# Kernel tuning notes

Measured on AMD Instinct MI355X. Metric: run time of the kernel, lower is better.

The kernel has to match this reference:

```python
import jax, jax.numpy as jnp
import numpy as np

B = 16384          # batch
F = 256            # num_features
H1, H2 = 32, 16    # hidden_units


def setup_inputs() -> dict:
    key = jax.random.key(0)
    ks = jax.random.split(key, 7)
    return {
        "x":  jax.random.normal(ks[0], (B, F), dtype=jnp.float32),
        "W1": jax.random.normal(ks[1], (F, 1, H1), dtype=jnp.float32) * 0.5,
        "b1": jax.random.normal(ks[2], (F, H1), dtype=jnp.float32) * 0.1,
        "W2": jax.random.normal(ks[3], (F, H1, H2), dtype=jnp.float32) * (1.0 / np.sqrt(H1)),
        "b2": jax.random.normal(ks[4], (F, H2), dtype=jnp.float32) * 0.1,
        "W3": jax.random.normal(ks[5], (F, H2, 1), dtype=jnp.float32) * (1.0 / np.sqrt(H2)),
        "b3": jax.random.normal(ks[6], (F, 1), dtype=jnp.float32) * 0.1,
    }


def reference(x, W1, b1, W2, b2, W3, b3):
    # Per-feature tiny MLP 1->H1->H2->1, batched over features as grouped GEMMs.
    # x: [B, F] (each feature is a scalar input to its own network)
    h1 = jax.nn.relu(jnp.einsum('bf,fh->bfh', x, W1[:, 0, :]) + b1)          # [B,F,H1]
    h2 = jax.nn.relu(jnp.einsum('bfh,fhk->bfk', h1, W2) + b2)                 # [B,F,H2]
    contrib = jnp.einsum('bfk,fk->bf', h2, W3[:, :, 0]) + b3[:, 0]           # [B,F]
    out = jnp.sum(contrib, axis=1, keepdims=True)                             # [B,1]
    return jax.nn.sigmoid(out)
```

## Files before the change

### kernel.cpp

```cpp
#include <hip/hip_runtime.h>
#include <math.h>

#define B_TOTAL 16384
#define F_TOTAL 256
#define H1 32
#define H2 16
#define FPB 16
#define RPB 256
#define REC 144

typedef _Float16 f16;
typedef __attribute__((ext_vector_type(2))) _Float16 f16x2;
typedef __attribute__((ext_vector_type(8))) _Float16 f16x8;
typedef __attribute__((ext_vector_type(4))) float floatx4;

union F8 { uint4 u; f16x2 h2[4]; f16x8 h8; };
union U1 { unsigned u; f16x2 h; };
union HU { f16 h; unsigned short u; };

__global__ __launch_bounds__(64) void nam_pack(
    const float* __restrict__ W1, const float* __restrict__ b1,
    const float* __restrict__ W2, const float* __restrict__ b2,
    const float* __restrict__ W3, const float* __restrict__ b3,
    uint4* __restrict__ pkR, float* __restrict__ b3sum)
{
    const int f = blockIdx.x;
    const int lane = threadIdx.x;
    const int n = lane & 15, q = lane >> 4;
    uint4* pF = pkR + (size_t)f * REC;

    F8 H, L;
    #pragma unroll
    for (int j = 0; j < 8; ++j) {
        float w = W2[(size_t)f * (H1 * H2) + (q * 8 + j) * H2 + n];
        f16 hi = (f16)w;
        H.h8[j] = hi;
        L.h8[j] = (f16)(w - (float)hi);
    }
    pF[lane] = H.u;
    pF[64 + lane] = L.u;

    if (n == 0) {
        F8 A, Bb;
        #pragma unroll
        for (int j = 0; j < 8; ++j) {
            A.h8[j]  = (f16)W1[(size_t)f * H1 + q * 8 + j];
            Bb.h8[j] = (f16)b1[(size_t)f * H1 + q * 8 + j];
        }
        pF[128 + q * 2] = A.u;
        pF[129 + q * 2] = Bb.u;
    }
    if (q == 0) {
        float2 e;
        e.x = b2[(size_t)f * H2 + n];
        e.y = W3[(size_t)f * H2 + n];
        ((float2*)(pF + 136))[n] = e;
    }
    if (f == 0) {
        float s = b3[lane] + b3[lane + 64] + b3[lane + 128] + b3[lane + 192];
        s += __shfl_xor(s, 1);
        s += __shfl_xor(s, 2);
        s += __shfl_xor(s, 4);
        s += __shfl_xor(s, 8);
        s += __shfl_xor(s, 16);
        s += __shfl_xor(s, 32);
        if (lane == 0) b3sum[0] = s;
    }
}

__global__ __launch_bounds__(256, 4) void nam_main(
    const float* __restrict__ x,
    const uint4* __restrict__ pkR,
    float* __restrict__ part)
{
    __shared__ uint4 fB[FPB * 128];
    __shared__ unsigned short xs_h[FPB * RPB];

    const int t = threadIdx.x;
    const int lane = t & 63;
    const int wave = t >> 6;
    const int n = lane & 15, q = lane >> 4;
    const int b0 = blockIdx.x * RPB;
    const int f0 = blockIdx.y * FPB;

    {
        const float4* xr = (const float4*)(x + (size_t)(b0 + t) * F_TOTAL + f0);
        #pragma unroll
        for (int i = 0; i < 4; ++i) {
            float4 v = xr[i];
            HU a, b, c, d;
            a.h = (f16)v.x; b.h = (f16)v.y; c.h = (f16)v.z; d.h = (f16)v.w;
            xs_h[(i * 4 + 0) * RPB + t] = a.u;
            xs_h[(i * 4 + 1) * RPB + t] = b.u;
            xs_h[(i * 4 + 2) * RPB + t] = c.u;
            xs_h[(i * 4 + 3) * RPB + t] = d.u;
        }
    }
    const uint4* pR = pkR + (size_t)f0 * REC;
    if (t < 128) {
        #pragma unroll
        for (int fi = 0; fi < FPB; ++fi)
            fB[fi * 128 + t] = pR[(size_t)fi * REC + t];
    }
    __syncthreads();

    uint4 Wv[2], Bv[2];
    float2 bwv[2];
    #pragma unroll
    for (int d = 0; d < 2; ++d) {
        const uint4* pF = pR + (size_t)d * REC;
        Wv[d]  = pF[128 + q * 2];
        Bv[d]  = pF[129 + q * 2];
        bwv[d] = ((const float2*)(pF + 136))[n];
    }

    floatx4 acc[4] = {{0.f,0.f,0.f,0.f},{0.f,0.f,0.f,0.f},
                      {0.f,0.f,0.f,0.f},{0.f,0.f,0.f,0.f}};
    const int rb = wave * 64;
    const f16x2 z2 = {(f16)0, (f16)0};

    #pragma unroll 2
    for (int fi = 0; fi < FPB; ++fi) {
        F8 W, Bi;
        W.u  = Wv[fi & 1];
        Bi.u = Bv[fi & 1];
        const float2 bw = bwv[fi & 1];

        const int nf = (fi + 2 < FPB) ? fi + 2 : fi;
        const uint4* pF = pR + (size_t)nf * REC;
        Wv[fi & 1]  = pF[128 + q * 2];
        Bv[fi & 1]  = pF[129 + q * 2];
        bwv[fi & 1] = ((const float2*)(pF + 136))[n];

        F8 Bh, Bl;
        Bh.u = fB[fi * 128 + lane];
        Bl.u = fB[fi * 128 + 64 + lane];

        #pragma unroll
        for (int m = 0; m < 4; ++m) {
            const unsigned short xu = xs_h[fi * RPB + rb + m * 16 + n];
            U1 xb; xb.u = ((unsigned)xu << 16) | xu;
            const f16x2 xp = xb.h;
            F8 A;
            #pragma unroll
            for (int tt = 0; tt < 4; ++tt) {
                f16x2 h = xp * W.h2[tt] + Bi.h2[tt];
                A.h2[tt] = __builtin_elementwise_max(h, z2);
            }
            floatx4 c = {0.f, 0.f, 0.f, 0.f};
            c = __builtin_amdgcn_mfma_f32_16x16x32_f16(A.h8, Bh.h8, c, 0, 0, 0);
            c = __builtin_amdgcn_mfma_f32_16x16x32_f16(A.h8, Bl.h8, c, 0, 0, 0);
            #pragma unroll
            for (int r = 0; r < 4; ++r) {
                float u = c[r] + bw.x;
                u = u > 0.f ? u : 0.f;
                acc[m][r] = fmaf(u, bw.y, acc[m][r]);
            }
        }
    }

    #pragma unroll
    for (int m = 0; m < 4; ++m) {
        #pragma unroll
        for (int r = 0; r < 4; ++r) {
            float v = acc[m][r];
            v += __shfl_xor(v, 1);
            v += __shfl_xor(v, 2);
            v += __shfl_xor(v, 4);
            v += __shfl_xor(v, 8);
            acc[m][r] = v;
        }
    }
    if (n == 0) {
        float* dst = part + (size_t)blockIdx.y * B_TOTAL + b0 + rb;
        #pragma unroll
        for (int m = 0; m < 4; ++m) {
            float4 o;
            o.x = acc[m][0]; o.y = acc[m][1];
            o.z = acc[m][2]; o.w = acc[m][3];
            *(float4*)(dst + m * 16 + q * 4) = o;
        }
    }
}

__global__ __launch_bounds__(256) void nam_finish(
    const float* __restrict__ part, const float* __restrict__ b3sum,
    float* __restrict__ out)
{
    const int b = blockIdx.x * 256 + threadIdx.x;
    float s = b3sum[0];
    #pragma unroll
    for (int g = 0; g < 16; ++g) s += part[(size_t)g * B_TOTAL + b];
    out[b] = 1.0f / (1.0f + expf(-s));
}

extern "C" void kernel_launch(void* const* d_in, const int* in_sizes, int n_in,
                              void* d_out, int out_size, void* d_ws, size_t ws_size,
                              hipStream_t stream) {
    const float* x  = (const float*)d_in[0];
    const float* W1 = (const float*)d_in[1];
    const float* b1 = (const float*)d_in[2];
    const float* W2 = (const float*)d_in[3];
    const float* b2 = (const float*)d_in[4];
    const float* W3 = (const float*)d_in[5];
    const float* b3 = (const float*)d_in[6];
    float* out = (float*)d_out;

    char* ws = (char*)d_ws;
    uint4* pkR   = (uint4*)ws;
    float* b3sum = (float*)(ws + (592 << 10));
    float* partp = (float*)(ws + (640 << 10));

    nam_pack<<<F_TOTAL, 64, 0, stream>>>(W1, b1, W2, b2, W3, b3, pkR, b3sum);

    dim3 grid(B_TOTAL / RPB, F_TOTAL / FPB);
    nam_main<<<grid, 256, 0, stream>>>(x, pkR, partp);

    nam_finish<<<B_TOTAL / 256, 256, 0, stream>>>(partp, b3sum, out);
}
```

Before: 94.68 us.

## Fuse pack, main and finish into one cooperative kernel with grid sync

```diff
diff --git a/kernel.cpp b/kernel.cpp
--- a/kernel.cpp
+++ b/kernel.cpp
@@ -1,13 +1,14 @@
 #include <hip/hip_runtime.h>
+#include <hip/hip_cooperative_groups.h>
 #include <math.h>
 
 #define B_TOTAL 16384
 #define F_TOTAL 256
 #define H1 32
 #define H2 16
-#define FPB 16
-#define RPB 256
-#define REC 144
+#define FPB 8
+#define RPB 512
+#define NG 32
 
 typedef _Float16 f16;
 typedef __attribute__((ext_vector_type(2))) _Float16 f16x2;
@@ -18,63 +19,19 @@
 union U1 { unsigned u; f16x2 h; };
 union HU { f16 h; unsigned short u; };
 
-__global__ __launch_bounds__(64) void nam_pack(
-    const float* __restrict__ W1, const float* __restrict__ b1,
-    const float* __restrict__ W2, const float* __restrict__ b2,
-    const float* __restrict__ W3, const float* __restrict__ b3,
-    uint4* __restrict__ pkR, float* __restrict__ b3sum)
-{
-    const int f = blockIdx.x;
-    const int lane = threadIdx.x;
-    const int n = lane & 15, q = lane >> 4;
-    uint4* pF = pkR + (size_t)f * REC;
-
-    F8 H, L;
-    #pragma unroll
-    for (int j = 0; j < 8; ++j) {
-        float w = W2[(size_t)f * (H1 * H2) + (q * 8 + j) * H2 + n];
-        f16 hi = (f16)w;
-        H.h8[j] = hi;
-        L.h8[j] = (f16)(w - (float)hi);
-    }
-    pF[lane] = H.u;
-    pF[64 + lane] = L.u;
-
-    if (n == 0) {
-        F8 A, Bb;
-        #pragma unroll
-        for (int j = 0; j < 8; ++j) {
-            A.h8[j]  = (f16)W1[(size_t)f * H1 + q * 8 + j];
-            Bb.h8[j] = (f16)b1[(size_t)f * H1 + q * 8 + j];
-        }
-        pF[128 + q * 2] = A.u;
-        pF[129 + q * 2] = Bb.u;
-    }
-    if (q == 0) {
-        float2 e;
-        e.x = b2[(size_t)f * H2 + n];
-        e.y = W3[(size_t)f * H2 + n];
-        ((float2*)(pF + 136))[n] = e;
-    }
-    if (f == 0) {
-        float s = b3[lane] + b3[lane + 64] + b3[lane + 128] + b3[lane + 192];
-        s += __shfl_xor(s, 1);
-        s += __shfl_xor(s, 2);
-        s += __shfl_xor(s, 4);
-        s += __shfl_xor(s, 8);
-        s += __shfl_xor(s, 16);
-        s += __shfl_xor(s, 32);
-        if (lane == 0) b3sum[0] = s;
-    }
-}
-
-__global__ __launch_bounds__(256, 4) void nam_main(
-    const float* __restrict__ x,
-    const uint4* __restrict__ pkR,
-    float* __restrict__ part)
+namespace cg = cooperative_groups;
+
+__device__ __forceinline__ void nam_phase1(
+    const float* __restrict__ x,   const float* __restrict__ W1,
+    const float* __restrict__ b1,  const float* __restrict__ W2,
+    const float* __restrict__ b2,  const float* __restrict__ W3,
+    const float* __restrict__ b3,  float* __restrict__ part)
 {
     __shared__ uint4 fB[FPB * 128];
     __shared__ unsigned short xs_h[FPB * RPB];
+    __shared__ uint4 w1b1s[FPB * 4 * 2];
+    __shared__ float2 bws[FPB * 16];
+    __shared__ float b3s[FPB];
 
     const int t = threadIdx.x;
     const int lane = t & 63;
@@ -83,61 +40,72 @@
     const int b0 = blockIdx.x * RPB;
     const int f0 = blockIdx.y * FPB;
 
-    {
-        const float4* xr = (const float4*)(x + (size_t)(b0 + t) * F_TOTAL + f0);
-        #pragma unroll
-        for (int i = 0; i < 4; ++i) {
+    #pragma unroll
+    for (int k = 0; k < 2; ++k) {
+        const int fi = wave * 2 + k;
+        const int f = f0 + fi;
+        F8 H, L;
+        #pragma unroll
+        for (int j = 0; j < 8; ++j) {
+            float w = W2[(size_t)f * (H1 * H2) + (q * 8 + j) * H2 + n];
+            f16 hi = (f16)w;
+            H.h8[j] = hi;
+            L.h8[j] = (f16)(w - (float)hi);
+        }
+        fB[fi * 128 + lane] = H.u;
+        fB[fi * 128 + 64 + lane] = L.u;
+        if (n == 0) {
+            F8 A, Bb;
+            #pragma unroll
+            for (int j = 0; j < 8; ++j) {
+                A.h8[j]  = (f16)W1[(size_t)f * H1 + q * 8 + j];
+                Bb.h8[j] = (f16)b1[(size_t)f * H1 + q * 8 + j];
+            }
+            w1b1s[(fi * 4 + q) * 2]     = A.u;
+            w1b1s[(fi * 4 + q) * 2 + 1] = Bb.u;
+        }
+        if (q == 0) {
+            float2 e;
+            e.x = b2[(size_t)f * H2 + n];
+            e.y = W3[(size_t)f * H2 + n];
+            bws[fi * 16 + n] = e;
+        }
+        if (lane == 0) b3s[fi] = b3[f];
+    }
+    #pragma unroll
+    for (int h = 0; h < 2; ++h) {
+        const int rr = t + h * 256;
+        const float4* xr = (const float4*)(x + (size_t)(b0 + rr) * F_TOTAL + f0);
+        #pragma unroll
+        for (int i = 0; i < 2; ++i) {
             float4 v = xr[i];
             HU a, b, c, d;
             a.h = (f16)v.x; b.h = (f16)v.y; c.h = (f16)v.z; d.h = (f16)v.w;
-            xs_h[(i * 4 + 0) * RPB + t] = a.u;
-            xs_h[(i * 4 + 1) * RPB + t] = b.u;
-            xs_h[(i * 4 + 2) * RPB + t] = c.u;
-            xs_h[(i * 4 + 3) * RPB + t] = d.u;
-        }
-    }
-    const uint4* pR = pkR + (size_t)f0 * REC;
-    if (t < 128) {
-        #pragma unroll
-        for (int fi = 0; fi < FPB; ++fi)
-            fB[fi * 128 + t] = pR[(size_t)fi * REC + t];
+            xs_h[(i * 4 + 0) * RPB + rr] = a.u;
+            xs_h[(i * 4 + 1) * RPB + rr] = b.u;
+            xs_h[(i * 4 + 2) * RPB + rr] = c.u;
+            xs_h[(i * 4 + 3) * RPB + rr] = d.u;
+        }
     }
     __syncthreads();
 
-    uint4 Wv[2], Bv[2];
-    float2 bwv[2];
-    #pragma unroll
-    for (int d = 0; d < 2; ++d) {
-        const uint4* pF = pR + (size_t)d * REC;
-        Wv[d]  = pF[128 + q * 2];
-        Bv[d]  = pF[129 + q * 2];
-        bwv[d] = ((const float2*)(pF + 136))[n];
-    }
-
-    floatx4 acc[4] = {{0.f,0.f,0.f,0.f},{0.f,0.f,0.f,0.f},
-                      {0.f,0.f,0.f,0.f},{0.f,0.f,0.f,0.f}};
-    const int rb = wave * 64;
+    floatx4 acc[8];
+    #pragma unroll
+    for (int m = 0; m < 8; ++m) acc[m] = (floatx4){0.f, 0.f, 0.f, 0.f};
+    const int rb = wave * 128;
     const f16x2 z2 = {(f16)0, (f16)0};
 
     #pragma unroll 2
     for (int fi = 0; fi < FPB; ++fi) {
-        F8 W, Bi;
-        W.u  = Wv[fi & 1];
-        Bi.u = Bv[fi & 1];
-        const float2 bw = bwv[fi & 1];
-
-        const int nf = (fi + 2 < FPB) ? fi + 2 : fi;
-        const uint4* pF = pR + (size_t)nf * REC;
-        Wv[fi & 1]  = pF[128 + q * 2];
-        Bv[fi & 1]  = pF[129 + q * 2];
-        bwv[fi & 1] = ((const float2*)(pF + 136))[n];
-
-        F8 Bh, Bl;
+        F8 Bh, Bl, W, Bi;
         Bh.u = fB[fi * 128 + lane];
         Bl.u = fB[fi * 128 + 64 + lane];
-
-        #pragma unroll
-        for (int m = 0; m < 4; ++m) {
+        W.u  = w1b1s[(fi * 4 + q) * 2];
+        Bi.u = w1b1s[(fi * 4 + q) * 2 + 1];
+        const float2 bw = bws[fi * 16 + n];
+
+        #pragma unroll
+        for (int m = 0; m < 8; ++m) {
             const unsigned short xu = xs_h[fi * RPB + rb + m * 16 + n];
             U1 xb; xb.u = ((unsigned)xu << 16) | xu;
             const f16x2 xp = xb.h;
@@ -159,8 +127,12 @@
         }
     }
 
-    #pragma unroll
-    for (int m = 0; m < 4; ++m) {
+    float accb3 = 0.f;
+    #pragma unroll
+    for (int i = 0; i < FPB; ++i) accb3 += b3s[i];
+
+    #pragma unroll
+    for (int m = 0; m < 8; ++m) {
         #pragma unroll
         for (int r = 0; r < 4; ++r) {
             float v = acc[m][r];
@@ -174,24 +146,63 @@
     if (n == 0) {
         float* dst = part + (size_t)blockIdx.y * B_TOTAL + b0 + rb;
         #pragma unroll
-        for (int m = 0; m < 4; ++m) {
-            float4 o;
-            o.x = acc[m][0]; o.y = acc[m][1];
-            o.z = acc[m][2]; o.w = acc[m][3];
-            *(float4*)(dst + m * 16 + q * 4) = o;
-        }
-    }
-}
-
-__global__ __launch_bounds__(256) void nam_finish(
-    const float* __restrict__ part, const float* __restrict__ b3sum,
+        for (int m = 0; m < 8; ++m) {
+            #pragma unroll
+            for (int r = 0; r < 4; ++r)
+                __hip_atomic_store(dst + m * 16 + q * 4 + r,
+                                   acc[m][r] + accb3,
+                                   __ATOMIC_RELAXED, __HIP_MEMORY_SCOPE_AGENT);
+        }
+    }
+}
+
+__device__ __forceinline__ void nam_phase2(
+    const float* __restrict__ part, float* __restrict__ out)
+{
+    __shared__ float red[256];
+    const int t = threadIdx.x;
+    const int flat = blockIdx.y * gridDim.x + blockIdx.x;
+    const int row = flat * 16 + (t & 15);
+    const int g0 = (t >> 4) * 2;
+    float p = __hip_atomic_load(part + (size_t)g0 * B_TOTAL + row,
+                                __ATOMIC_RELAXED, __HIP_MEMORY_SCOPE_AGENT)
+            + __hip_atomic_load(part + (size_t)(g0 + 1) * B_TOTAL + row,
+                                __ATOMIC_RELAXED, __HIP_MEMORY_SCOPE_AGENT);
+    red[t] = p;
+    __syncthreads();
+    if (t < 16) {
+        float s = 0.f;
+        #pragma unroll
+        for (int i = 0; i < 16; ++i) s += red[i * 16 + t];
+        out[flat * 16 + t] = 1.0f / (1.0f + expf(-s));
+    }
+}
+
+__global__ __launch_bounds__(256, 4) void nam_coop(
+    const float* __restrict__ x,  const float* __restrict__ W1,
+    const float* __restrict__ b1, const float* __restrict__ W2,
+    const float* __restrict__ b2, const float* __restrict__ W3,
+    const float* __restrict__ b3, float* __restrict__ part,
     float* __restrict__ out)
 {
-    const int b = blockIdx.x * 256 + threadIdx.x;
-    float s = b3sum[0];
-    #pragma unroll
-    for (int g = 0; g < 16; ++g) s += part[(size_t)g * B_TOTAL + b];
-    out[b] = 1.0f / (1.0f + expf(-s));
+    nam_phase1(x, W1, b1, W2, b2, W3, b3, part);
+    cg::this_grid().sync();
+    nam_phase2(part, out);
+}
+
+__global__ __launch_bounds__(256, 4) void nam_p1(
+    const float* __restrict__ x,  const float* __restrict__ W1,
+    const float* __restrict__ b1, const float* __restrict__ W2,
+    const float* __restrict__ b2, const float* __restrict__ W3,
+    const float* __restrict__ b3, float* __restrict__ part)
+{
+    nam_phase1(x, W1, b1, W2, b2, W3, b3, part);
+}
+
+__global__ __launch_bounds__(256, 4) void nam_p2(
+    const float* __restrict__ part, float* __restrict__ out)
+{
+    nam_phase2(part, out);
 }
 
 extern "C" void kernel_launch(void* const* d_in, const int* in_sizes, int n_in,
@@ -205,16 +216,18 @@
     const float* W3 = (const float*)d_in[5];
     const float* b3 = (const float*)d_in[6];
     float* out = (float*)d_out;
-
-    char* ws = (char*)d_ws;
-    uint4* pkR   = (uint4*)ws;
-    float* b3sum = (float*)(ws + (592 << 10));
-    float* partp = (float*)(ws + (640 << 10));
-
-    nam_pack<<<F_TOTAL, 64, 0, stream>>>(W1, b1, W2, b2, W3, b3, pkR, b3sum);
-
-    dim3 grid(B_TOTAL / RPB, F_TOTAL / FPB);
-    nam_main<<<grid, 256, 0, stream>>>(x, pkR, partp);
-
-    nam_finish<<<B_TOTAL / 256, 256, 0, stream>>>(partp, b3sum, out);
-}
+    float* part = (float*)d_ws;
+
+    dim3 grid(B_TOTAL / RPB, NG);
+    dim3 block(256);
+
+    void* args[] = {(void*)&x, (void*)&W1, (void*)&b1, (void*)&W2,
+                    (void*)&b2, (void*)&W3, (void*)&b3, (void*)&part,
+                    (void*)&out};
+    hipError_t err = hipLaunchCooperativeKernel(
+        (const void*)nam_coop, grid, block, args, 0, stream);
+    if (err != hipSuccess) {
+        nam_p1<<<grid, block, 0, stream>>>(x, W1, b1, W2, b2, W3, b3, part);
+        nam_p2<<<grid, block, 0, stream>>>(part, out);
+    }
+}
```

Result: slower. 221.9 us (+134.4%).
